# Kernel optimization log

Measured on AMD Instinct MI355X. Metric: run time of the kernel, lower is better.

The kernel has to match this reference:

```python
import jax, jax.numpy as jnp
import numpy as np

B, IN, OUT = 4096, 1024, 1024


def setup_inputs() -> dict:
    key = jax.random.key(0)
    ks = jax.random.split(key, 11)
    xav = 1.0 / np.sqrt(IN + OUT)  # Xavier-style scale for sigmoid/tanh layers
    d = {
        "x": jax.random.normal(ks[0], (B, IN), dtype=jnp.float32),
        "h": jax.random.normal(ks[1], (B, OUT), dtype=jnp.float32),
        "c": jax.random.normal(ks[2], (B, OUT), dtype=jnp.float32),
        "w_f": jax.random.normal(ks[3], (IN + OUT, OUT), dtype=jnp.float32) * xav,
        "b_f": jnp.zeros((1, OUT), dtype=jnp.float32),
        "w_i": jax.random.normal(ks[4], (IN + OUT, OUT), dtype=jnp.float32) * xav,
        "b_i": jnp.zeros((1, OUT), dtype=jnp.float32),
        "w_c": jax.random.normal(ks[5], (IN + OUT, OUT), dtype=jnp.float32) * xav,
        "b_c": jnp.zeros((1, OUT), dtype=jnp.float32),
        "w_o": jax.random.normal(ks[6], (IN + OUT, OUT), dtype=jnp.float32) * xav,
        "b_o": jnp.zeros((1, OUT), dtype=jnp.float32),
    }
    return d


def reference(x, h, c, w_f, b_f, w_i, b_i, w_c, b_c, w_o, b_o):
    # combined input [B, IN+OUT]
    z = jnp.concatenate([x, h], axis=1)
    f = jax.nn.sigmoid(z @ w_f + b_f)      # forget gate
    i = jax.nn.sigmoid(z @ w_i + b_i)      # update (input) gate
    g = jnp.tanh(z @ w_c + b_c)            # candidate cell
    o = jax.nn.sigmoid(z @ w_o + b_o)      # output gate
    c_new = c * f + i * g
    h_new = jnp.tanh(c_new) * o
    return h_new
```

## Files before the change

kernel.cpp:

```cpp
#include <hip/hip_runtime.h>
#include <hip/hip_bf16.h>

typedef short short8 __attribute__((ext_vector_type(8)));
typedef float f32x4 __attribute__((ext_vector_type(4)));

#define NB 4096
#define KZ 2048
#define NG 1024
#define NSTEP 64

__device__ __forceinline__ unsigned short f2bf(float f) {
  unsigned int u = __float_as_uint(f);
  u += 0x7FFFu + ((u >> 16) & 1u);
  return (unsigned short)(u >> 16);
}
__device__ __forceinline__ float bf2f(unsigned short s) {
  return __uint_as_float(((unsigned int)s) << 16);
}
__device__ __forceinline__ void gload_lds16(const void* g, void* l) {
  __builtin_amdgcn_global_load_lds(
      (__attribute__((address_space(1))) void*)g,
      (__attribute__((address_space(3))) void*)l, 16, 0, 0);
}
__device__ __forceinline__ float sigm(float x) { return 1.f / (1.f + __expf(-x)); }
__device__ __forceinline__ float tanh_fast(float x) {
  float e = __expf(-2.f * fabsf(x));
  float r = (1.f - e) / (1.f + e);
  return copysignf(r, x);
}

__global__ void zsplit_kernel(const float* __restrict__ x, const float* __restrict__ h,
                              unsigned short* __restrict__ zh) {
  int idx = blockIdx.x * 256 + threadIdx.x;
  int e = idx << 2;
  int r = e >> 11;
  int k = e & (KZ - 1);
  const float* src = (k < 1024) ? (x + ((size_t)r << 10) + k)
                                : (h + ((size_t)r << 10) + (k - 1024));
  float4 v = *reinterpret_cast<const float4*>(src);
  float vf[4] = {v.x, v.y, v.z, v.w};
  unsigned short hh[4];
#pragma unroll
  for (int j = 0; j < 4; ++j) hh[j] = f2bf(vf[j]);
  uint2 H = make_uint2((unsigned)hh[0] | ((unsigned)hh[1] << 16),
                       (unsigned)hh[2] | ((unsigned)hh[3] << 16));
  *reinterpret_cast<uint2*>(zh + e) = H;
}

__global__ void wsplit_kernel(const float* __restrict__ w0, const float* __restrict__ w1,
                              const float* __restrict__ w2, const float* __restrict__ w3,
                              unsigned short* __restrict__ wh, unsigned short* __restrict__ wl) {
  __shared__ float tile[32][33];
  int g = blockIdx.z;
  const float* w = (g == 0) ? w0 : (g == 1) ? w1 : (g == 2) ? w2 : w3;
  int k0 = blockIdx.x << 5;
  int n0 = blockIdx.y << 5;
  int t = threadIdx.x;
  int rk = t >> 3, q = t & 7;
  float4 v = *reinterpret_cast<const float4*>(w + (size_t)(k0 + rk) * NG + n0 + (q << 2));
  tile[rk][(q << 2) + 0] = v.x;
  tile[rk][(q << 2) + 1] = v.y;
  tile[rk][(q << 2) + 2] = v.z;
  tile[rk][(q << 2) + 3] = v.w;
  __syncthreads();
  int n = t >> 3, kq = t & 7;
  unsigned short hs[4], ls[4];
#pragma unroll
  for (int j = 0; j < 4; ++j) {
    float f = tile[(kq << 2) + j][n];
    unsigned short hi = f2bf(f);
    unsigned short lo = f2bf(f - bf2f(hi));
    hs[j] = hi; ls[j] = lo;
  }
  int nn = n0 + n;
  int p = ((nn >> 6) << 8) | (((nn >> 4) & 3) << 6) | (g << 4) | (nn & 15);
  size_t o = (size_t)p * KZ + k0 + (kq << 2);
  uint2 H = make_uint2((unsigned)hs[0] | ((unsigned)hs[1] << 16),
                       (unsigned)hs[2] | ((unsigned)hs[3] << 16));
  uint2 L = make_uint2((unsigned)ls[0] | ((unsigned)ls[1] << 16),
                       (unsigned)ls[2] | ((unsigned)ls[3] << 16));
  *reinterpret_cast<uint2*>(wh + o) = H;
  *reinterpret_cast<uint2*>(wl + o) = L;
}

#define MFMA(a, b, c) __builtin_amdgcn_mfma_f32_16x16x32_bf16((a), (b), (c), 0, 0, 0)
#define BAR() __builtin_amdgcn_s_barrier()
#define LGKM(N) asm volatile("s_waitcnt lgkmcnt(" #N ")" ::: "memory")
#define VMC(N) asm volatile("s_waitcnt vmcnt(" #N ")" ::: "memory")
#define SB() __builtin_amdgcn_sched_barrier(0)
#define PRIO1() __builtin_amdgcn_s_setprio(1)
#define PRIO0() __builtin_amdgcn_s_setprio(0)

__global__ __launch_bounds__(512, 2) void lstm_gemm_kernel(
    const unsigned short* __restrict__ zh,
    const unsigned short* __restrict__ wh, const unsigned short* __restrict__ wl,
    const float* __restrict__ c_in, const float* __restrict__ bf_,
    const float* __restrict__ bi_, const float* __restrict__ bc_,
    const float* __restrict__ bo_, float* __restrict__ out) {
  __shared__ unsigned short As[2 * 8192];
  __shared__ unsigned short Bhs[3 * 8192];
  __shared__ unsigned short Bls[3 * 8192];
  const int t = threadIdx.x;
  const int lane = t & 63;
  const int wid = t >> 6;
  const int wr = wid >> 2;
  const int wc = wid & 3;
  const int l15 = lane & 15;
  const int l4 = lane >> 4;

  const int bid = blockIdx.x;
  const int xcd = bid & 7;
  const int i = bid >> 3;
  const int bxc = (xcd << 1) | (i & 1);
  const int byr = i >> 1;
  const int brow0 = byr << 7;
  const int pcol0 = bxc << 8;

  char* AsB = (char*)As;
  char* BhB = (char*)Bhs;
  char* BlB = (char*)Bls;

  int aoffA[2], boffB[2];
#pragma unroll
  for (int j = 0; j < 2; ++j) {
    int ra = (j << 6) + (t >> 3);
    aoffA[j] = (brow0 + ra) * KZ + (((t & 7) ^ (ra & 7)) << 3);
    int rb2 = (j << 7) + (t >> 2);
    boffB[j] = (pcol0 + rb2) * KZ + (((t & 3) ^ ((rb2 >> 1) & 3)) << 3);
  }

  auto STAGE_A = [&](int m) {
    const int p = (m & 1) << 14;
    const int kb = m << 6;
#pragma unroll
    for (int j = 0; j < 2; ++j)
      gload_lds16(zh + aoffA[j] + kb, AsB + p + (j << 13) + (t << 4));
  };
  auto STAGE_B = [&](int s, int b) {
    const int kb = s << 5;
    const int bb = b << 14;
#pragma unroll
    for (int j = 0; j < 2; ++j) {
      gload_lds16(wh + boffB[j] + kb, BhB + bb + (j << 13) + (t << 4));
      gload_lds16(wl + boffB[j] + kb, BlB + bb + (j << 13) + (t << 4));
    }
  };

  f32x4 acc[4][4];
#pragma unroll
  for (int mt = 0; mt < 4; ++mt)
#pragma unroll
    for (int nf = 0; nf < 4; ++nf) acc[mt][nf] = (f32x4){0.f, 0.f, 0.f, 0.f};

  const int rxA = l15 & 7;
  const int aRow = (wr << 13) + (l15 << 7);
  const int sxB = (l4 ^ ((l15 >> 1) & 3)) << 4;
  const int bRow = (wc << 12) + (l15 << 6) + sxB;

  short8 a[4], bh[4], bl[4];

  STAGE_A(0); STAGE_B(0, 0); STAGE_B(1, 1);
  VMC(4);
  BAR();

  int rb = 0, sb = 2;
  for (int s = 0; s < NSTEP; ++s) {
    const int h = s & 1;
    const int ap = ((s >> 1) & 1) << 14;
    const int sxA = (((h << 2) + l4) ^ rxA) << 4;
    const int bbase = rb << 14;

#pragma unroll
    for (int mt = 0; mt < 4; ++mt)
      a[mt] = *reinterpret_cast<const short8*>(AsB + ap + aRow + (mt << 11) + sxA);
#pragma unroll
    for (int nf = 0; nf < 4; ++nf)
      bh[nf] = *reinterpret_cast<const short8*>(BhB + bbase + bRow + (nf << 10));
    SB();
#pragma unroll
    for (int nf = 0; nf < 4; ++nf)
      bl[nf] = *reinterpret_cast<const short8*>(BlB + bbase + bRow + (nf << 10));
    SB();

    if (s < NSTEP - 2) {
      STAGE_B(s + 2, sb);
      if (h == 0) STAGE_A((s >> 1) + 1);
    }

    LGKM(4); SB();
    PRIO1();
#pragma unroll
    for (int mt = 0; mt < 4; ++mt)
#pragma unroll
      for (int nf = 0; nf < 4; ++nf) acc[mt][nf] = MFMA(a[mt], bh[nf], acc[mt][nf]);
    PRIO0();
    LGKM(0); SB();
    PRIO1();
#pragma unroll
    for (int mt = 0; mt < 4; ++mt)
#pragma unroll
      for (int nf = 0; nf < 4; ++nf) acc[mt][nf] = MFMA(a[mt], bl[nf], acc[mt][nf]);
    PRIO0();

    if (s < NSTEP - 2) {
      if (h) { VMC(4); } else { VMC(6); }
    } else {
      VMC(0);
    }
    SB();
    BAR();
    rb = (rb == 2) ? 0 : rb + 1;
    sb = (sb == 2) ? 0 : sb + 1;
  }

  const int ng = (bxc << 6) + (wc << 4) + l15;
  const float vbf = bf_[ng], vbi = bi_[ng], vbc = bc_[ng], vbo = bo_[ng];
#pragma unroll
  for (int mt = 0; mt < 4; ++mt) {
#pragma unroll
    for (int r = 0; r < 4; ++r) {
      const int row = brow0 + (wr << 6) + (mt << 4) + (l4 << 2) + r;
      const float fp = acc[mt][0][r] + vbf;
      const float ip = acc[mt][1][r] + vbi;
      const float gp = acc[mt][2][r] + vbc;
      const float op = acc[mt][3][r] + vbo;
      const float co = c_in[(size_t)row * NG + ng];
      const float cnew = co * sigm(fp) + sigm(ip) * tanh_fast(gp);
      out[(size_t)row * NG + ng] = tanh_fast(cnew) * sigm(op);
    }
  }
}

extern "C" void kernel_launch(void* const* d_in, const int* in_sizes, int n_in,
                              void* d_out, int out_size, void* d_ws, size_t ws_size,
                              hipStream_t stream) {
  const float* x   = (const float*)d_in[0];
  const float* h   = (const float*)d_in[1];
  const float* c   = (const float*)d_in[2];
  const float* w_f = (const float*)d_in[3];
  const float* b_f = (const float*)d_in[4];
  const float* w_i = (const float*)d_in[5];
  const float* b_i = (const float*)d_in[6];
  const float* w_c = (const float*)d_in[7];
  const float* b_c = (const float*)d_in[8];
  const float* w_o = (const float*)d_in[9];
  const float* b_o = (const float*)d_in[10];
  float* out = (float*)d_out;

  unsigned short* zh = (unsigned short*)d_ws;
  unsigned short* wh = zh + (size_t)NB * KZ;
  unsigned short* wl = wh + (size_t)KZ * 4096;

  zsplit_kernel<<<(NB * KZ / 4) / 256, 256, 0, stream>>>(x, h, zh);
  wsplit_kernel<<<dim3(KZ / 32, NG / 32, 4), 256, 0, stream>>>(w_f, w_i, w_c, w_o, wh, wl);
  lstm_gemm_kernel<<<512, 512, 0, stream>>>(zh, wh, wl, c,
                                            b_f, b_i, b_c, b_o, out);
}
```

Before: 151.6 us.

## Double block M tile to 256 rows with register double-buffered B fragments

Each workgroup now covers 256 batch rows instead of 128, so the grid halves and every B (weight hi/lo) tile loaded into LDS is reused across twice as many rows. The schedule moves from a triple-buffered B ring to a double-buffered LDS scheme with B fragments prefetched into registers between the hi and lo MFMA passes. The XOR swizzle on B tiles is removed from both the global staging and the LDS reads. In exchange, the accumulators and register buffers roughly double, which risks spills or lower occupancy under the existing launch bounds. The removed swizzle may also bring back LDS bank conflicts, and the 256-block grid gives about one block per CU.

Measured after the change: 134.1 us. 11.5% less time.

```diff
diff --git a/kernel.cpp b/kernel.cpp
--- a/kernel.cpp
+++ b/kernel.cpp
@@ -7,7 +7,7 @@
 #define NB 4096
 #define KZ 2048
 #define NG 1024
-#define NSTEP 64
+#define NH 64
 
 __device__ __forceinline__ unsigned short f2bf(float f) {
   unsigned int u = __float_as_uint(f);
@@ -85,7 +85,7 @@
 
 #define MFMA(a, b, c) __builtin_amdgcn_mfma_f32_16x16x32_bf16((a), (b), (c), 0, 0, 0)
 #define BAR() __builtin_amdgcn_s_barrier()
-#define LGKM(N) asm volatile("s_waitcnt lgkmcnt(" #N ")" ::: "memory")
+#define LGKM0() asm volatile("s_waitcnt lgkmcnt(0)" ::: "memory")
 #define VMC(N) asm volatile("s_waitcnt vmcnt(" #N ")" ::: "memory")
 #define SB() __builtin_amdgcn_sched_barrier(0)
 #define PRIO1() __builtin_amdgcn_s_setprio(1)
@@ -97,9 +97,9 @@
     const float* __restrict__ c_in, const float* __restrict__ bf_,
     const float* __restrict__ bi_, const float* __restrict__ bc_,
     const float* __restrict__ bo_, float* __restrict__ out) {
-  __shared__ unsigned short As[2 * 8192];
-  __shared__ unsigned short Bhs[3 * 8192];
-  __shared__ unsigned short Bls[3 * 8192];
+  __shared__ unsigned short As[2 * 16384];
+  __shared__ unsigned short Bhs[2 * 8192];
+  __shared__ unsigned short Bls[2 * 8192];
   const int t = threadIdx.x;
   const int lane = t & 63;
   const int wid = t >> 6;
@@ -113,117 +113,127 @@
   const int i = bid >> 3;
   const int bxc = (xcd << 1) | (i & 1);
   const int byr = i >> 1;
-  const int brow0 = byr << 7;
+  const int brow0 = byr << 8;
   const int pcol0 = bxc << 8;
 
   char* AsB = (char*)As;
   char* BhB = (char*)Bhs;
   char* BlB = (char*)Bls;
 
-  int aoffA[2], boffB[2];
-#pragma unroll
-  for (int j = 0; j < 2; ++j) {
+  int aoffA[4];
+#pragma unroll
+  for (int j = 0; j < 4; ++j) {
     int ra = (j << 6) + (t >> 3);
     aoffA[j] = (brow0 + ra) * KZ + (((t & 7) ^ (ra & 7)) << 3);
-    int rb2 = (j << 7) + (t >> 2);
-    boffB[j] = (pcol0 + rb2) * KZ + (((t & 3) ^ ((rb2 >> 1) & 3)) << 3);
-  }
-
-  auto STAGE_A = [&](int m) {
-    const int p = (m & 1) << 14;
+  }
+  int boffB[2];
+#pragma unroll
+  for (int j = 0; j < 2; ++j)
+    boffB[j] = (pcol0 + (j << 7) + (t >> 2)) * KZ + ((t & 3) << 3);
+
+  auto ASTAGE = [&](int m) {
     const int kb = m << 6;
-#pragma unroll
-    for (int j = 0; j < 2; ++j)
+    const int p = (m & 1) << 15;
+#pragma unroll
+    for (int j = 0; j < 4; ++j)
       gload_lds16(zh + aoffA[j] + kb, AsB + p + (j << 13) + (t << 4));
   };
-  auto STAGE_B = [&](int s, int b) {
-    const int kb = s << 5;
-    const int bb = b << 14;
-#pragma unroll
-    for (int j = 0; j < 2; ++j) {
-      gload_lds16(wh + boffB[j] + kb, BhB + bb + (j << 13) + (t << 4));
-      gload_lds16(wl + boffB[j] + kb, BlB + bb + (j << 13) + (t << 4));
-    }
+  auto BSTAGE = [&](int hh) {
+    const int kb = hh << 5;
+    const int p = (hh & 1) << 14;
+#pragma unroll
+    for (int j = 0; j < 2; ++j)
+      gload_lds16(wh + boffB[j] + kb, BhB + p + (j << 13) + (t << 4));
+#pragma unroll
+    for (int j = 0; j < 2; ++j)
+      gload_lds16(wl + boffB[j] + kb, BlB + p + (j << 13) + (t << 4));
   };
 
-  f32x4 acc[4][4];
-#pragma unroll
-  for (int mt = 0; mt < 4; ++mt)
-#pragma unroll
-    for (int nf = 0; nf < 4; ++nf) acc[mt][nf] = (f32x4){0.f, 0.f, 0.f, 0.f};
-
-  const int rxA = l15 & 7;
-  const int aRow = (wr << 13) + (l15 << 7);
-  const int sxB = (l4 ^ ((l15 >> 1) & 3)) << 4;
-  const int bRow = (wc << 12) + (l15 << 6) + sxB;
-
-  short8 a[4], bh[4], bl[4];
-
-  STAGE_A(0); STAGE_B(0, 0); STAGE_B(1, 1);
-  VMC(4);
+  f32x4 acc[8][4];
+#pragma unroll
+  for (int m = 0; m < 8; ++m)
+#pragma unroll
+    for (int n = 0; n < 4; ++n) acc[m][n] = (f32x4){0.f, 0.f, 0.f, 0.f};
+
+  const int rx = l15 & 7;
+  const int aRow = (wr << 14) + (l15 << 7);
+  const int sxA0 = (l4 ^ rx) << 4;
+  const int sxA1 = ((4 + l4) ^ rx) << 4;
+  const int bRow = (wc << 12) + (l15 << 6) + (l4 << 4);
+
+  short8 a[8], bhA[4], blA[4], bhB[4], blB[4];
+
+  ASTAGE(0); BSTAGE(0); BSTAGE(1);
+  VMC(4); SB();
   BAR();
-
-  int rb = 0, sb = 2;
-  for (int s = 0; s < NSTEP; ++s) {
-    const int h = s & 1;
-    const int ap = ((s >> 1) & 1) << 14;
-    const int sxA = (((h << 2) + l4) ^ rxA) << 4;
-    const int bbase = rb << 14;
-
-#pragma unroll
-    for (int mt = 0; mt < 4; ++mt)
-      a[mt] = *reinterpret_cast<const short8*>(AsB + ap + aRow + (mt << 11) + sxA);
-#pragma unroll
-    for (int nf = 0; nf < 4; ++nf)
-      bh[nf] = *reinterpret_cast<const short8*>(BhB + bbase + bRow + (nf << 10));
-    SB();
-#pragma unroll
-    for (int nf = 0; nf < 4; ++nf)
-      bl[nf] = *reinterpret_cast<const short8*>(BlB + bbase + bRow + (nf << 10));
-    SB();
-
-    if (s < NSTEP - 2) {
-      STAGE_B(s + 2, sb);
-      if (h == 0) STAGE_A((s >> 1) + 1);
-    }
-
-    LGKM(4); SB();
-    PRIO1();
-#pragma unroll
-    for (int mt = 0; mt < 4; ++mt)
-#pragma unroll
-      for (int nf = 0; nf < 4; ++nf) acc[mt][nf] = MFMA(a[mt], bh[nf], acc[mt][nf]);
-    PRIO0();
-    LGKM(0); SB();
-    PRIO1();
-#pragma unroll
-    for (int mt = 0; mt < 4; ++mt)
-#pragma unroll
-      for (int nf = 0; nf < 4; ++nf) acc[mt][nf] = MFMA(a[mt], bl[nf], acc[mt][nf]);
-    PRIO0();
-
-    if (s < NSTEP - 2) {
-      if (h) { VMC(4); } else { VMC(6); }
-    } else {
-      VMC(0);
-    }
-    SB();
-    BAR();
-    rb = (rb == 2) ? 0 : rb + 1;
-    sb = (sb == 2) ? 0 : sb + 1;
+#pragma unroll
+  for (int nf = 0; nf < 4; ++nf) {
+    bhA[nf] = *reinterpret_cast<const short8*>(BhB + bRow + (nf << 10));
+    blA[nf] = *reinterpret_cast<const short8*>(BlB + bRow + (nf << 10));
+  }
+  VMC(0); SB();
+  LGKM0(); SB();
+  BAR();
+
+#define HALF_BODY(H, HP, SX, APAR, CBH, CBL, NBH, NBL, EVMC)                    \
+  {                                                                             \
+    _Pragma("unroll")                                                           \
+    for (int m = 0; m < 8; ++m)                                                 \
+      a[m] = *reinterpret_cast<const short8*>(AsB + ((APAR) << 15) + aRow +     \
+                                              (m << 11) + (SX));                \
+    if ((H) + 2 < NH) BSTAGE((H) + 2);                                          \
+    if ((((H) & 1) == 0) && ((HP) + 1 < 32)) ASTAGE((HP) + 1);                  \
+    SB();                                                                       \
+    PRIO1();                                                                    \
+    _Pragma("unroll")                                                           \
+    for (int m = 0; m < 8; ++m) {                                               \
+      acc[m][0] = MFMA(a[m], CBH[0], acc[m][0]);                                \
+      acc[m][1] = MFMA(a[m], CBH[1], acc[m][1]);                                \
+      acc[m][2] = MFMA(a[m], CBH[2], acc[m][2]);                                \
+      acc[m][3] = MFMA(a[m], CBH[3], acc[m][3]);                                \
+    }                                                                           \
+    PRIO0();                                                                    \
+    SB();                                                                       \
+    if ((H) + 1 < NH) {                                                         \
+      const int np = (((H) + 1) & 1) << 14;                                     \
+      _Pragma("unroll")                                                         \
+      for (int nf = 0; nf < 4; ++nf) {                                          \
+        NBH[nf] = *reinterpret_cast<const short8*>(BhB + np + bRow + (nf << 10));\
+        NBL[nf] = *reinterpret_cast<const short8*>(BlB + np + bRow + (nf << 10));\
+      }                                                                         \
+    }                                                                           \
+    SB();                                                                       \
+    PRIO1();                                                                    \
+    _Pragma("unroll")                                                           \
+    for (int m = 0; m < 8; ++m) {                                               \
+      acc[m][0] = MFMA(a[m], CBL[0], acc[m][0]);                                \
+      acc[m][1] = MFMA(a[m], CBL[1], acc[m][1]);                                \
+      acc[m][2] = MFMA(a[m], CBL[2], acc[m][2]);                                \
+      acc[m][3] = MFMA(a[m], CBL[3], acc[m][3]);                                \
+    }                                                                           \
+    PRIO0();                                                                    \
+    VMC(EVMC); SB();                                                            \
+    LGKM0(); SB();                                                              \
+    BAR();                                                                      \
+  }
+
+  for (int hp = 0; hp < 32; ++hp) {
+    const int apar = hp & 1;
+    HALF_BODY(2 * hp,     hp, sxA0, apar, bhA, blA, bhB, blB, 4);
+    HALF_BODY(2 * hp + 1, hp, sxA1, apar, bhB, blB, bhA, blA, 0);
   }
 
   const int ng = (bxc << 6) + (wc << 4) + l15;
   const float vbf = bf_[ng], vbi = bi_[ng], vbc = bc_[ng], vbo = bo_[ng];
 #pragma unroll
-  for (int mt = 0; mt < 4; ++mt) {
+  for (int m = 0; m < 8; ++m) {
 #pragma unroll
     for (int r = 0; r < 4; ++r) {
-      const int row = brow0 + (wr << 6) + (mt << 4) + (l4 << 2) + r;
-      const float fp = acc[mt][0][r] + vbf;
-      const float ip = acc[mt][1][r] + vbi;
-      const float gp = acc[mt][2][r] + vbc;
-      const float op = acc[mt][3][r] + vbo;
+      const int row = brow0 + (wr << 7) + (m << 4) + (l4 << 2) + r;
+      const float fp = acc[m][0][r] + vbf;
+      const float ip = acc[m][1][r] + vbi;
+      const float gp = acc[m][2][r] + vbc;
+      const float op = acc[m][3][r] + vbo;
       const float co = c_in[(size_t)row * NG + ng];
       const float cnew = co * sigm(fp) + sigm(ip) * tanh_fast(gp);
       out[(size_t)row * NG + ng] = tanh_fast(cnew) * sigm(op);
@@ -253,6 +263,6 @@
 
   zsplit_kernel<<<(NB * KZ / 4) / 256, 256, 0, stream>>>(x, h, zh);
   wsplit_kernel<<<dim3(KZ / 32, NG / 32, 4), 256, 0, stream>>>(w_f, w_i, w_c, w_o, wh, wl);
-  lstm_gemm_kernel<<<512, 512, 0, stream>>>(zh, wh, wl, c,
+  lstm_gemm_kernel<<<256, 512, 0, stream>>>(zh, wh, wl, c,
                                             b_f, b_i, b_c, b_o, out);
 }
```
